# Optimization experiments

Measured on AMD Instinct MI355X. Metric: run time of the kernel, lower is better.

The kernel has to match this reference:

```python
import jax, jax.numpy as jnp
import numpy as np

B = 16384      # batch of states
N = 64         # neighbors per state -> x width = 5 + 2*N = 133
H = 128        # embed / hidden feature dim (num_inputs)
HID = 256      # actor/critic hidden size
OUT = 2        # action dim


def setup_inputs() -> dict:
    key = jax.random.key(0)
    ks = jax.random.split(key, 12)
    w = lambda k, shp: (jax.random.normal(k, shp, jnp.float32) * 0.1)
    b = lambda n: jnp.full((n,), 0.1, jnp.float32)
    return {
        "x": jax.random.normal(ks[0], (B, 5 + 2 * N), jnp.float32),
        # embbedLayer: Linear(2,128)
        "We": w(ks[1], (H, 2)), "be": b(H),
        # hlayer: Linear(128,128)
        "Wh": w(ks[2], (H, H)), "bh": b(H),
        # attentionLayer: Linear(256,1)
        "Wa": w(ks[3], (1, 2 * H)), "ba": b(1),
        # layer2: Linear(133,128)
        "W2": w(ks[4], (H, H + 5)), "b2": b(H),
        # critic: Linear(128,256) -> Linear(256,1)
        "Wc1": w(ks[5], (HID, H)), "bc1": b(HID),
        "Wc2": w(ks[6], (1, HID)), "bc2": b(1),
        # actor: Linear(128,256) -> Linear(256,2)
        "Wp1": w(ks[7], (HID, H)), "bp1": b(HID),
        "Wp2": w(ks[8], (OUT, HID)), "bp2": b(OUT),
        # log_std parameter (std=0.0 -> ones*0.0)
        "log_std": jnp.zeros((1, OUT), jnp.float32),
    }


def reference(x, We, be, Wh, bh, Wa, ba, W2, b2,
              Wc1, bc1, Wc2, bc2, Wp1, bp1, Wp2, bp2, log_std):
    Bn = x.shape[0]
    state_loc = x[:, :5]                       # [B,5]
    nb = x[:, 5:].reshape(Bn, -1, 2)           # [B,N,2] ragged loop flattened

    e = jax.nn.relu(jnp.einsum('bnd,hd->bnh', nb, We) + be)   # [B,N,H]
    em = jnp.mean(e, axis=1, keepdims=True)                    # [B,1,H]
    h = jax.nn.relu(jnp.einsum('bnh,oh->bno', e, Wh) + bh)     # [B,N,H]

    # attentionLayer(hstack(e, em)): split Wa into e-part and mean-part
    Wa_e, Wa_m = Wa[:, :H], Wa[:, H:]
    score = jax.nn.relu(
        jnp.einsum('bnh,oh->bno', e, Wa_e)
        + jnp.einsum('bkh,oh->bko', em, Wa_m)   # [B,1,1] broadcasts over N
        + ba
    )                                            # [B,N,1]
    attn = jax.nn.softmax(score, axis=1)         # softmax over neighbors
    mean_feature = jnp.mean(attn * h, axis=1)    # [B,H]

    t = jax.nn.relu(
        jnp.concatenate([state_loc, mean_feature], axis=1) @ W2.T + b2
    )                                            # [B,H]

    value = jax.nn.relu(t @ Wc1.T + bc1) @ Wc2.T + bc2   # [B,1]
    mu = jax.nn.relu(t @ Wp1.T + bp1) @ Wp2.T + bp2       # [B,2]
    std = jnp.broadcast_to(jnp.exp(log_std), mu.shape)    # [B,2]
    return mu, std, value
```

## Files before the change

### kernel.cpp

```cpp
#include <hip/hip_runtime.h>

#define BATCH 16384
#define XDIM  133
#define RPB   2
#define EROW  272
#define MB    64
#define CROW  336
#define TROW  272

#define WH_OFF   0
#define W2_OFF   16384
#define WC1_OFF  36864
#define WP1_OFF  69632
#define WA_OFF   102400
#define WE2_OFF  102528
#define MFG_OFF  208896

typedef __attribute__((ext_vector_type(8))) _Float16 half8;
typedef __attribute__((ext_vector_type(4))) _Float16 half4v;
typedef __attribute__((ext_vector_type(2))) _Float16 half2v;
typedef __attribute__((ext_vector_type(4))) float    f32x4;
typedef __attribute__((ext_vector_type(4))) unsigned int uint4v;

__device__ __forceinline__ float relu(float v) { return fmaxf(v, 0.f); }
__device__ __forceinline__ unsigned short f2h(float f) {
    _Float16 h = (_Float16)f;
    return __builtin_bit_cast(unsigned short, h);
}
__device__ __forceinline__ half2v pk2h(float a, float b) {
    return __builtin_bit_cast(half2v, __builtin_amdgcn_cvt_pkrtz(a, b));
}

__global__ __launch_bounds__(256)
void ac_prep(const float* __restrict__ Wh, const float* __restrict__ W2,
             const float* __restrict__ Wc1, const float* __restrict__ Wp1,
             const float* __restrict__ Wa, const float* __restrict__ We,
             const float* __restrict__ be, unsigned short* __restrict__ wsH)
{
    const int idx = blockIdx.x * 256 + threadIdx.x;
    const int stride = gridDim.x * 256;
    for (int i = idx; i < 128*128; i += stride) wsH[WH_OFF + i] = f2h(Wh[i]);
    for (int i = idx; i < 128*160; i += stride) {
        int o = i / 160, ck = i - o*160;
        float w = (ck < 128) ? W2[o*XDIM + 5 + ck]
                             : ((ck < 133) ? W2[o*XDIM + (ck - 128)] : 0.f);
        wsH[W2_OFF + i] = f2h(w);
    }
    for (int i = idx; i < 256*128; i += stride) wsH[WC1_OFF + i] = f2h(Wc1[i]);
    for (int i = idx; i < 256*128; i += stride) wsH[WP1_OFF + i] = f2h(Wp1[i]);
    for (int i = idx; i < 128;     i += stride) wsH[WA_OFF  + i] = f2h(Wa[i]);
    for (int hp = idx; hp < 128;   hp += stride) {
        wsH[WE2_OFF + hp*8 + 0] = f2h(We[4*hp+0]);
        wsH[WE2_OFF + hp*8 + 1] = f2h(We[4*hp+2]);
        wsH[WE2_OFF + hp*8 + 2] = f2h(We[4*hp+1]);
        wsH[WE2_OFF + hp*8 + 3] = f2h(We[4*hp+3]);
        wsH[WE2_OFF + hp*8 + 4] = f2h(be[2*hp+0]);
        wsH[WE2_OFF + hp*8 + 5] = f2h(be[2*hp+1]);
        wsH[WE2_OFF + hp*8 + 6] = f2h(Wa[128+2*hp+0]);
        wsH[WE2_OFF + hp*8 + 7] = f2h(Wa[128+2*hp+1]);
    }
}

__global__ __launch_bounds__(512, 8)
void ac_attn(const float* __restrict__ x,
             const float* __restrict__ bh,  const float* __restrict__ ba,
             const unsigned short* __restrict__ wsH,
             char* __restrict__ mfG)
{
    __shared__ __align__(16) char  eH[RPB * 64 * EROW];
    __shared__ __align__(16) char  xsH[RPB * 64 * 8];
    __shared__ __align__(16) float attnS[RPB][64];
    __shared__ __align__(16) float pS[8][64];
    __shared__            float cpart[8];

    const int tid  = threadIdx.x;
    const int lane = tid & 63;
    const int wave = tid >> 6;
    const int b0   = blockIdx.x * RPB;

    if (tid < 128) {
        int r = tid >> 6, n = tid & 63;
        float2 nb = *(const float2*)(x + (size_t)(b0 + r) * XDIM + 5 + 2*n);
        half2v s0 = pk2h(nb.x, nb.x);
        half2v s1 = pk2h(nb.y, nb.y);
        half4v s; s[0] = s0[0]; s[1] = s0[1]; s[2] = s1[0]; s[3] = s1[1];
        *(half4v*)(xsH + (r*64 + n)*8) = s;
    }
    __syncthreads();

    {
        const int hp = lane;
        const int r  = wave >> 2;
        const int nq = wave & 3;
        half8 wp = *(const half8*)(wsH + WE2_OFF + hp*8);
        half2v W0 = {wp[0], wp[1]};
        half2v W1 = {wp[2], wp[3]};
        half2v BE = {wp[4], wp[5]};
        half2v WAM = {wp[6], wp[7]};
        const half2v Z = {(_Float16)0.0f, (_Float16)0.0f};
        float ca = 0.f;
        #pragma unroll
        for (int i = 0; i < 16; ++i) {
            int n = nq*16 + i;
            half4v s = *(const half4v*)(xsH + (r*64 + n)*8);
            half2v s0 = {s[0], s[1]};
            half2v s1 = {s[2], s[3]};
            half2v X = s0*W0 + BE;
            X = s1*W1 + X;
            X = __builtin_elementwise_max(X, Z);
            ca = __builtin_amdgcn_fdot2(X, WAM, ca, false);
            *(half2v*)(eH + (r*64 + n)*EROW + (hp << 2)) = X;
        }
        #pragma unroll
        for (int off = 1; off < 64; off <<= 1) ca += __shfl_xor(ca, off);
        if (lane == 0) cpart[wave] = ca;
    }
    __syncthreads();

    {
        const int r  = wave & 1;
        const int kq = wave >> 1;
        const int n  = lane;
        const int row = r*64 + n;
        const half2v* wa = (const half2v*)(wsH + WA_OFF) + kq*16;
        float s = 0.f;
        #pragma unroll
        for (int k16 = 0; k16 < 4; ++k16) {
            half8 v = *(const half8*)(eH + row*EROW + kq*64 + k16*16);
            const half2v* v2 = (const half2v*)&v;
            #pragma unroll
            for (int j = 0; j < 4; ++j)
                s = __builtin_amdgcn_fdot2(v2[j], wa[k16*4 + j], s, false);
        }
        pS[wave][n] = s;
    }
    __syncthreads();

    if (wave < 2) {
        const int r = wave;
        const int n = lane;
        float s = pS[r][n] + pS[2 + r][n] + pS[4 + r][n] + pS[6 + r][n];
        float c = (cpart[r*4+0] + cpart[r*4+1] + cpart[r*4+2] + cpart[r*4+3]) * (1.f/64.f) + ba[0];
        float sc = relu(s + c);
        float m = sc;
        #pragma unroll
        for (int off = 1; off < 64; off <<= 1) m = fmaxf(m, __shfl_xor(m, off));
        float p = __expf(sc - m);
        float sum = p;
        #pragma unroll
        for (int off = 1; off < 64; off <<= 1) sum += __shfl_xor(sum, off);
        attnS[r][n] = p / (sum * 64.f);
    }
    __syncthreads();

    {
        const int lo = lane & 15;
        const int g  = lane >> 4;
        const int c0 = wave*16 + lo;
        const unsigned short* WhH = wsH + WH_OFF;
        half8 bfr[4];
        #pragma unroll
        for (int kk = 0; kk < 4; ++kk)
            bfr[kk] = *(const half8*)(WhH + c0*128 + kk*32 + g*8);
        const float bh0 = bh[c0];

        #pragma unroll
        for (int r = 0; r < RPB; ++r) {
            float mfp = 0.f;
            #pragma unroll
            for (int nt = 0; nt < 4; ++nt) {
                const int arow = r*64 + nt*16 + lo;
                f32x4 acc = {0.f, 0.f, 0.f, 0.f};
                #pragma unroll
                for (int kk = 0; kk < 4; ++kk) {
                    half8 af = *(const half8*)(eH + arow*EROW + kk*64 + g*16);
                    acc = __builtin_amdgcn_mfma_f32_16x16x32_f16(af, bfr[kk], acc, 0, 0, 0);
                }
                f32x4 at4 = *(const f32x4*)&attnS[r][nt*16 + g*4];
                #pragma unroll
                for (int j = 0; j < 4; ++j)
                    mfp = fmaf(at4[j], relu(acc[j] + bh0), mfp);
            }
            mfp += __shfl_xor(mfp, 16);
            mfp += __shfl_xor(mfp, 32);
            if (lane < 16)
                *(unsigned short*)(mfG + ((size_t)(b0 + r) * 128 + wave*16 + lane) * 2) = f2h(mfp);
        }
    }
}

__global__ __launch_bounds__(256, 1)
void ac_heads(const float* __restrict__ x, const char* __restrict__ mfG,
              const unsigned short* __restrict__ wsH,
              const float* __restrict__ b2,
              const float* __restrict__ bc1, const float* __restrict__ Wc2,
              const float* __restrict__ bc2,
              const float* __restrict__ bp1, const float* __restrict__ Wp2,
              const float* __restrict__ bp2,
              const float* __restrict__ log_std,
              float* __restrict__ out)
{
    __shared__ __align__(16) char catS[MB * CROW];
    __shared__ __align__(16) char tS[MB * TROW];
    __shared__ float redV [2][MB];
    __shared__ float redM0[2][MB];
    __shared__ float redM1[2][MB];

    const int tid  = threadIdx.x;
    const int lane = tid & 63;
    const int wave = tid >> 6;
    const int lo   = lane & 15;
    const int g    = lane >> 4;
    const int b0   = blockIdx.x * MB;

    for (int i = tid * 16; i < MB * CROW; i += 256 * 16)
        *(uint4v*)(catS + i) = (uint4v){0, 0, 0, 0};
    __syncthreads();
    for (int c = tid; c < MB * 16; c += 256) {
        int row = c >> 4, sl = c & 15;
        uint4v v = *(const uint4v*)(mfG + (size_t)(b0 + row) * 256 + sl * 16);
        *(uint4v*)(catS + row * CROW + sl * 16) = v;
    }
    for (int m = tid; m < MB; m += 256) {
        const float* xr = x + (size_t)(b0 + m) * XDIM;
        #pragma unroll
        for (int k = 0; k < 5; ++k)
            *(unsigned short*)(catS + m * CROW + 256 + 2*k) = f2h(xr[k]);
    }
    __syncthreads();

    {
        const int o = wave * 32 + lo;
        const unsigned short* W2H = wsH + W2_OFF;
        half8 bw[2][5];
        #pragma unroll
        for (int nt2 = 0; nt2 < 2; ++nt2)
            #pragma unroll
            for (int kk = 0; kk < 5; ++kk)
                bw[nt2][kk] = *(const half8*)(W2H + (size_t)(o + nt2*16)*160 + kk*32 + g*8);
        const float bb0 = b2[o], bb1 = b2[o + 16];
        #pragma unroll
        for (int mt = 0; mt < 4; ++mt) {
            const int arow = mt*16 + lo;
            half8 af[5];
            #pragma unroll
            for (int kk = 0; kk < 5; ++kk)
                af[kk] = *(const half8*)(catS + arow*CROW + kk*64 + g*16);
            f32x4 a0 = {0.f,0.f,0.f,0.f}, a1 = {0.f,0.f,0.f,0.f};
            #pragma unroll
            for (int kk = 0; kk < 5; ++kk) {
                a0 = __builtin_amdgcn_mfma_f32_16x16x32_f16(af[kk], bw[0][kk], a0, 0, 0, 0);
                a1 = __builtin_amdgcn_mfma_f32_16x16x32_f16(af[kk], bw[1][kk], a1, 0, 0, 0);
            }
            #pragma unroll
            for (int j = 0; j < 4; ++j) {
                int m = mt*16 + g*4 + j;
                *(unsigned short*)(tS + m*TROW + o*2)      = f2h(relu(a0[j] + bb0));
                *(unsigned short*)(tS + m*TROW + (o+16)*2) = f2h(relu(a1[j] + bb1));
            }
        }
    }
    __syncthreads();

    {
        const bool isval = (wave < 2);
        const unsigned short* W1H = wsH + (isval ? WC1_OFF : WP1_OFF);
        const float* bb = isval ? bc1 : bp1;
        const int obase = (wave & 1) * 128;
        float sA[4][4], sB[4][4];
        #pragma unroll
        for (int mt = 0; mt < 4; ++mt)
            #pragma unroll
            for (int j = 0; j < 4; ++j) { sA[mt][j] = 0.f; sB[mt][j] = 0.f; }

        #pragma unroll
        for (int np = 0; np < 4; ++np) {
            const int oA = obase + np*32 + lo;
            const int oB = oA + 16;
            half8 bf0[4], bf1[4];
            #pragma unroll
            for (int kk = 0; kk < 4; ++kk) {
                bf0[kk] = *(const half8*)(W1H + (size_t)oA*128 + kk*32 + g*8);
                bf1[kk] = *(const half8*)(W1H + (size_t)oB*128 + kk*32 + g*8);
            }
            const float biasA = bb[oA], biasB = bb[oB];
            float wA0, wB0, wA1 = 0.f, wB1 = 0.f;
            if (isval) { wA0 = Wc2[oA]; wB0 = Wc2[oB]; }
            else       { wA0 = Wp2[oA]; wB0 = Wp2[oB]; wA1 = Wp2[256+oA]; wB1 = Wp2[256+oB]; }

            #pragma unroll
            for (int mt = 0; mt < 4; ++mt) {
                const int arow = mt*16 + lo;
                half8 af[4];
                #pragma unroll
                for (int kk = 0; kk < 4; ++kk)
                    af[kk] = *(const half8*)(tS + arow*TROW + kk*64 + g*16);
                f32x4 a0 = {0.f,0.f,0.f,0.f}, a1 = {0.f,0.f,0.f,0.f};
                #pragma unroll
                for (int kk = 0; kk < 4; ++kk) {
                    a0 = __builtin_amdgcn_mfma_f32_16x16x32_f16(af[kk], bf0[kk], a0, 0, 0, 0);
                    a1 = __builtin_amdgcn_mfma_f32_16x16x32_f16(af[kk], bf1[kk], a1, 0, 0, 0);
                }
                #pragma unroll
                for (int j = 0; j < 4; ++j) {
                    float uA = relu(a0[j] + biasA);
                    float uB = relu(a1[j] + biasB);
                    sA[mt][j] += wA0*uA + wB0*uB;
                    sB[mt][j] += wA1*uA + wB1*uB;
                }
            }
        }
        #pragma unroll
        for (int mt = 0; mt < 4; ++mt)
            #pragma unroll
            for (int j = 0; j < 4; ++j) {
                #pragma unroll
                for (int off = 1; off < 16; off <<= 1) {
                    sA[mt][j] += __shfl_xor(sA[mt][j], off);
                    sB[mt][j] += __shfl_xor(sB[mt][j], off);
                }
            }
        if (lo == 0) {
            #pragma unroll
            for (int mt = 0; mt < 4; ++mt)
                #pragma unroll
                for (int j = 0; j < 4; ++j) {
                    int m = mt*16 + g*4 + j;
                    if (isval) redV[wave][m] = sA[mt][j];
                    else { redM0[wave-2][m] = sA[mt][j]; redM1[wave-2][m] = sB[mt][j]; }
                }
        }
    }
    __syncthreads();

    if (tid < MB) {
        const int m = tid;
        const int b = b0 + m;
        out[b*2 + 0]           = redM0[0][m] + redM0[1][m] + bp2[0];
        out[b*2 + 1]           = redM1[0][m] + redM1[1][m] + bp2[1];
        out[2*BATCH + b*2 + 0] = expf(log_std[0]);
        out[2*BATCH + b*2 + 1] = expf(log_std[1]);
        out[4*BATCH + b]       = redV[0][m] + redV[1][m] + bc2[0];
    }
}

extern "C" void kernel_launch(void* const* d_in, const int* in_sizes, int n_in,
                              void* d_out, int out_size, void* d_ws, size_t ws_size,
                              hipStream_t stream) {
    (void)in_sizes; (void)n_in; (void)ws_size; (void)out_size;
    const float* x       = (const float*)d_in[0];
    const float* We      = (const float*)d_in[1];
    const float* be      = (const float*)d_in[2];
    const float* Wh      = (const float*)d_in[3];
    const float* bh      = (const float*)d_in[4];
    const float* Wa      = (const float*)d_in[5];
    const float* ba      = (const float*)d_in[6];
    const float* W2      = (const float*)d_in[7];
    const float* b2      = (const float*)d_in[8];
    const float* Wc1     = (const float*)d_in[9];
    const float* bc1     = (const float*)d_in[10];
    const float* Wc2     = (const float*)d_in[11];
    const float* bc2     = (const float*)d_in[12];
    const float* Wp1     = (const float*)d_in[13];
    const float* bp1     = (const float*)d_in[14];
    const float* Wp2     = (const float*)d_in[15];
    const float* bp2     = (const float*)d_in[16];
    const float* log_std = (const float*)d_in[17];

    unsigned short* wsH = (unsigned short*)d_ws;
    char* mfG = (char*)d_ws + MFG_OFF;

    hipLaunchKernelGGL(ac_prep, dim3(64), dim3(256), 0, stream,
                       Wh, W2, Wc1, Wp1, Wa, We, be, wsH);
    hipLaunchKernelGGL(ac_attn, dim3(BATCH / RPB), dim3(512), 0, stream,
                       x, bh, ba, wsH, mfG);
    hipLaunchKernelGGL(ac_heads, dim3(BATCH / MB), dim3(256), 0, stream,
                       x, mfG, wsH, b2, bc1, Wc2, bc2, bp1, Wp2, bp2,
                       log_std, (float*)d_out);
}
```

Measured before the change: 83.95 us.

## Fuse attention scoring and online softmax into the MFMA pass in ac_attn

```diff
diff --git a/kernel.cpp b/kernel.cpp
--- a/kernel.cpp
+++ b/kernel.cpp
@@ -17,7 +17,6 @@
 #define MFG_OFF  208896
 
 typedef __attribute__((ext_vector_type(8))) _Float16 half8;
-typedef __attribute__((ext_vector_type(4))) _Float16 half4v;
 typedef __attribute__((ext_vector_type(2))) _Float16 half2v;
 typedef __attribute__((ext_vector_type(4))) float    f32x4;
 typedef __attribute__((ext_vector_type(4))) unsigned int uint4v;
@@ -61,50 +60,38 @@
     }
 }
 
-__global__ __launch_bounds__(512, 8)
+__global__ __launch_bounds__(256, 4)
 void ac_attn(const float* __restrict__ x,
              const float* __restrict__ bh,  const float* __restrict__ ba,
              const unsigned short* __restrict__ wsH,
              char* __restrict__ mfG)
 {
     __shared__ __align__(16) char  eH[RPB * 64 * EROW];
-    __shared__ __align__(16) char  xsH[RPB * 64 * 8];
-    __shared__ __align__(16) float attnS[RPB][64];
-    __shared__ __align__(16) float pS[8][64];
-    __shared__            float cpart[8];
+    __shared__            float cpart[4];
 
     const int tid  = threadIdx.x;
     const int lane = tid & 63;
     const int wave = tid >> 6;
     const int b0   = blockIdx.x * RPB;
 
-    if (tid < 128) {
-        int r = tid >> 6, n = tid & 63;
-        float2 nb = *(const float2*)(x + (size_t)(b0 + r) * XDIM + 5 + 2*n);
-        half2v s0 = pk2h(nb.x, nb.x);
-        half2v s1 = pk2h(nb.y, nb.y);
-        half4v s; s[0] = s0[0]; s[1] = s0[1]; s[2] = s1[0]; s[3] = s1[1];
-        *(half4v*)(xsH + (r*64 + n)*8) = s;
-    }
-    __syncthreads();
-
     {
         const int hp = lane;
-        const int r  = wave >> 2;
-        const int nq = wave & 3;
+        const int r  = wave >> 1;
+        const int nh = wave & 1;
         half8 wp = *(const half8*)(wsH + WE2_OFF + hp*8);
         half2v W0 = {wp[0], wp[1]};
         half2v W1 = {wp[2], wp[3]};
         half2v BE = {wp[4], wp[5]};
         half2v WAM = {wp[6], wp[7]};
         const half2v Z = {(_Float16)0.0f, (_Float16)0.0f};
+        const float* xr = x + (size_t)(b0 + r) * XDIM + 5;
         float ca = 0.f;
         #pragma unroll
-        for (int i = 0; i < 16; ++i) {
-            int n = nq*16 + i;
-            half4v s = *(const half4v*)(xsH + (r*64 + n)*8);
-            half2v s0 = {s[0], s[1]};
-            half2v s1 = {s[2], s[3]};
+        for (int i = 0; i < 32; ++i) {
+            int n = nh*32 + i;
+            float2 nb = *(const float2*)(xr + 2*n);
+            half2v s0 = pk2h(nb.x, nb.x);
+            half2v s1 = pk2h(nb.y, nb.y);
             half2v X = s0*W0 + BE;
             X = s1*W1 + X;
             X = __builtin_elementwise_max(X, Z);
@@ -118,73 +105,105 @@
     __syncthreads();
 
     {
-        const int r  = wave & 1;
-        const int kq = wave >> 1;
-        const int n  = lane;
-        const int row = r*64 + n;
-        const half2v* wa = (const half2v*)(wsH + WA_OFF) + kq*16;
-        float s = 0.f;
-        #pragma unroll
-        for (int k16 = 0; k16 < 4; ++k16) {
-            half8 v = *(const half8*)(eH + row*EROW + kq*64 + k16*16);
-            const half2v* v2 = (const half2v*)&v;
-            #pragma unroll
-            for (int j = 0; j < 4; ++j)
-                s = __builtin_amdgcn_fdot2(v2[j], wa[k16*4 + j], s, false);
-        }
-        pS[wave][n] = s;
-    }
-    __syncthreads();
-
-    if (wave < 2) {
-        const int r = wave;
-        const int n = lane;
-        float s = pS[r][n] + pS[2 + r][n] + pS[4 + r][n] + pS[6 + r][n];
-        float c = (cpart[r*4+0] + cpart[r*4+1] + cpart[r*4+2] + cpart[r*4+3]) * (1.f/64.f) + ba[0];
-        float sc = relu(s + c);
-        float m = sc;
-        #pragma unroll
-        for (int off = 1; off < 64; off <<= 1) m = fmaxf(m, __shfl_xor(m, off));
-        float p = __expf(sc - m);
-        float sum = p;
-        #pragma unroll
-        for (int off = 1; off < 64; off <<= 1) sum += __shfl_xor(sum, off);
-        attnS[r][n] = p / (sum * 64.f);
-    }
-    __syncthreads();
-
-    {
         const int lo = lane & 15;
         const int g  = lane >> 4;
-        const int c0 = wave*16 + lo;
+        const int r  = wave >> 1;
+        const int ch = wave & 1;
         const unsigned short* WhH = wsH + WH_OFF;
-        half8 bfr[4];
+
+        half8 bfr[4][4];
+        float bhr[4];
+        #pragma unroll
+        for (int ct = 0; ct < 4; ++ct) {
+            const int c = ch*64 + ct*16 + lo;
+            #pragma unroll
+            for (int kk = 0; kk < 4; ++kk)
+                bfr[ct][kk] = *(const half8*)(WhH + c*128 + kk*32 + g*8);
+            bhr[ct] = bh[c];
+        }
+        const half8 hz = {(_Float16)0.f,(_Float16)0.f,(_Float16)0.f,(_Float16)0.f,
+                          (_Float16)0.f,(_Float16)0.f,(_Float16)0.f,(_Float16)0.f};
+        half8 bsc[4];
         #pragma unroll
         for (int kk = 0; kk < 4; ++kk)
-            bfr[kk] = *(const half8*)(WhH + c0*128 + kk*32 + g*8);
-        const float bh0 = bh[c0];
-
-        #pragma unroll
-        for (int r = 0; r < RPB; ++r) {
-            float mfp = 0.f;
-            #pragma unroll
-            for (int nt = 0; nt < 4; ++nt) {
-                const int arow = r*64 + nt*16 + lo;
-                f32x4 acc = {0.f, 0.f, 0.f, 0.f};
-                #pragma unroll
-                for (int kk = 0; kk < 4; ++kk) {
-                    half8 af = *(const half8*)(eH + arow*EROW + kk*64 + g*16);
-                    acc = __builtin_amdgcn_mfma_f32_16x16x32_f16(af, bfr[kk], acc, 0, 0, 0);
-                }
-                f32x4 at4 = *(const f32x4*)&attnS[r][nt*16 + g*4];
-                #pragma unroll
-                for (int j = 0; j < 4; ++j)
-                    mfp = fmaf(at4[j], relu(acc[j] + bh0), mfp);
-            }
-            mfp += __shfl_xor(mfp, 16);
-            mfp += __shfl_xor(mfp, 32);
-            if (lane < 16)
-                *(unsigned short*)(mfG + ((size_t)(b0 + r) * 128 + wave*16 + lane) * 2) = f2h(mfp);
+            bsc[kk] = (lo == 0) ? *(const half8*)(wsH + WA_OFF + kk*32 + g*8) : hz;
+
+        const float cterm = (cpart[r*2] + cpart[r*2+1]) * (1.f/64.f) + ba[0];
+
+        float m = 0.f, lsum = 0.f;
+        float mfv[4] = {0.f, 0.f, 0.f, 0.f};
+
+        #pragma unroll
+        for (int nt = 0; nt < 4; ++nt) {
+            const int arow = r*64 + nt*16 + lo;
+            half8 af[4];
+            #pragma unroll
+            for (int kk = 0; kk < 4; ++kk)
+                af[kk] = *(const half8*)(eH + arow*EROW + kk*64 + g*16);
+
+            f32x4 sac = {0.f,0.f,0.f,0.f};
+            #pragma unroll
+            for (int kk = 0; kk < 4; ++kk)
+                sac = __builtin_amdgcn_mfma_f32_16x16x32_f16(af[kk], bsc[kk], sac, 0, 0, 0);
+            float s_[4];
+            #pragma unroll
+            for (int j = 0; j < 4; ++j) s_[j] = relu(sac[j] + cterm);
+            #pragma unroll
+            for (int j = 0; j < 4; ++j) s_[j] = __shfl(s_[j], lane & 48);
+
+            f32x4 acc0 = {0.f,0.f,0.f,0.f}, acc1 = {0.f,0.f,0.f,0.f};
+            f32x4 acc2 = {0.f,0.f,0.f,0.f}, acc3 = {0.f,0.f,0.f,0.f};
+            #pragma unroll
+            for (int kk = 0; kk < 4; ++kk) {
+                acc0 = __builtin_amdgcn_mfma_f32_16x16x32_f16(af[kk], bfr[0][kk], acc0, 0, 0, 0);
+                acc1 = __builtin_amdgcn_mfma_f32_16x16x32_f16(af[kk], bfr[1][kk], acc1, 0, 0, 0);
+                acc2 = __builtin_amdgcn_mfma_f32_16x16x32_f16(af[kk], bfr[2][kk], acc2, 0, 0, 0);
+                acc3 = __builtin_amdgcn_mfma_f32_16x16x32_f16(af[kk], bfr[3][kk], acc3, 0, 0, 0);
+            }
+
+            float pm = fmaxf(fmaxf(s_[0], s_[1]), fmaxf(s_[2], s_[3]));
+            float mn = fmaxf(m, pm);
+            float resc = __expf(m - mn);
+            lsum *= resc;
+            #pragma unroll
+            for (int ct = 0; ct < 4; ++ct) mfv[ct] *= resc;
+            float p_[4];
+            #pragma unroll
+            for (int j = 0; j < 4; ++j) p_[j] = __expf(s_[j] - mn);
+            lsum += p_[0] + p_[1] + p_[2] + p_[3];
+            #pragma unroll
+            for (int j = 0; j < 4; ++j) {
+                mfv[0] = fmaf(p_[j], relu(acc0[j] + bhr[0]), mfv[0]);
+                mfv[1] = fmaf(p_[j], relu(acc1[j] + bhr[1]), mfv[1]);
+                mfv[2] = fmaf(p_[j], relu(acc2[j] + bhr[2]), mfv[2]);
+                mfv[3] = fmaf(p_[j], relu(acc3[j] + bhr[3]), mfv[3]);
+            }
+            m = mn;
+        }
+
+        #pragma unroll
+        for (int off = 16; off <= 32; off <<= 1) {
+            float mo  = __shfl_xor(m, off);
+            float lo_ = __shfl_xor(lsum, off);
+            float f0  = __shfl_xor(mfv[0], off);
+            float f1  = __shfl_xor(mfv[1], off);
+            float f2  = __shfl_xor(mfv[2], off);
+            float f3  = __shfl_xor(mfv[3], off);
+            float mn = fmaxf(m, mo);
+            float a = __expf(m - mn), b = __expf(mo - mn);
+            lsum  = lsum*a + lo_*b;
+            mfv[0] = mfv[0]*a + f0*b;
+            mfv[1] = mfv[1]*a + f1*b;
+            mfv[2] = mfv[2]*a + f2*b;
+            mfv[3] = mfv[3]*a + f3*b;
+            m = mn;
+        }
+        const float inv = 1.0f / (lsum * 64.f);
+        if (g == 0) {
+            #pragma unroll
+            for (int ct = 0; ct < 4; ++ct)
+                *(unsigned short*)(mfG + ((size_t)(b0 + r)*128 + ch*64 + ct*16 + lo)*2)
+                    = f2h(mfv[ct] * inv);
         }
     }
 }
@@ -372,7 +391,7 @@
 
     hipLaunchKernelGGL(ac_prep, dim3(64), dim3(256), 0, stream,
                        Wh, W2, Wc1, Wp1, Wa, We, be, wsH);
-    hipLaunchKernelGGL(ac_attn, dim3(BATCH / RPB), dim3(512), 0, stream,
+    hipLaunchKernelGGL(ac_attn, dim3(BATCH / RPB), dim3(256), 0, stream,
                        x, bh, ba, wsH, mfG);
     hipLaunchKernelGGL(ac_heads, dim3(BATCH / MB), dim3(256), 0, stream,
                        x, mfG, wsH, b2, bc1, Wc2, bc2, bp1, Wp2, bp2,
```

Result: slower. 216.6 us (+158.0%).
